# Kernel optimization log

Measured on AMD Instinct MI355X. Metric: run time of the kernel, lower is better.

## Reference

```python
import jax, jax.numpy as jnp
import numpy as np

B, T, F = 8192, 30, 16
H1, H2 = 64, 32


def _lstm(x, Wih, Whh, b):
    """PyTorch-convention LSTM (gate order i,f,g,o). x: [B,T,I] -> (ys [B,T,H], hT [B,H])."""
    H = Whh.shape[1]
    h0 = jnp.zeros((x.shape[0], H), x.dtype)

    def step(carry, xt):
        h, c = carry
        z = xt @ Wih.T + h @ Whh.T + b  # [B,4H]
        i, f, g, o = jnp.split(z, 4, axis=-1)
        c = jax.nn.sigmoid(f) * c + jax.nn.sigmoid(i) * jnp.tanh(g)
        h = jax.nn.sigmoid(o) * jnp.tanh(c)
        return (h, c), h

    (hT, _), ys = jax.lax.scan(step, (h0, h0), jnp.swapaxes(x, 0, 1))
    return jnp.swapaxes(ys, 0, 1), hT


def setup_inputs() -> dict:
    key = jax.random.key(0)
    ks = jax.random.split(key, 16)
    s = 0.1  # small init scale for numerical sanity
    return {
        "x": jax.random.normal(ks[0], (B, T, F), jnp.float32),
        "Wih1": jax.random.normal(ks[1], (4 * H1, F), jnp.float32) * s,
        "Whh1": jax.random.normal(ks[2], (4 * H1, H1), jnp.float32) * s,
        "b1": jax.random.normal(ks[3], (4 * H1,), jnp.float32) * s,
        "Wih2": jax.random.normal(ks[4], (4 * H2, H1), jnp.float32) * s,
        "Whh2": jax.random.normal(ks[5], (4 * H2, H2), jnp.float32) * s,
        "b2": jax.random.normal(ks[6], (4 * H2,), jnp.float32) * s,
        "Wih3": jax.random.normal(ks[7], (4 * H2, H2), jnp.float32) * s,
        "Whh3": jax.random.normal(ks[8], (4 * H2, H2), jnp.float32) * s,
        "b3": jax.random.normal(ks[9], (4 * H2,), jnp.float32) * s,
        "Wih4": jax.random.normal(ks[10], (4 * H1, H2), jnp.float32) * s,
        "Whh4": jax.random.normal(ks[11], (4 * H1, H1), jnp.float32) * s,
        "b4": jax.random.normal(ks[12], (4 * H1,), jnp.float32) * s,
        "Wout": jax.random.normal(ks[13], (F, H1), jnp.float32) * s,
        "bout": jax.random.normal(ks[14], (F,), jnp.float32) * s,
    }


def reference(x, Wih1, Whh1, b1, Wih2, Whh2, b2, Wih3, Whh3, b3, Wih4, Whh4, b4, Wout, bout):
    ys1, _ = _lstm(x, Wih1, Whh1, b1)          # encoder LSTM(64)
    _, latent = _lstm(ys1, Wih2, Whh2, b2)      # encoder LSTM(32) -> final hidden [B,32]
    repeated = jnp.broadcast_to(latent[:, None, :], (latent.shape[0], T, latent.shape[1]))
    ys3, _ = _lstm(repeated, Wih3, Whh3, b3)    # decoder LSTM(32)
    ys4, _ = _lstm(ys3, Wih4, Whh4, b4)         # decoder LSTM(64)
    return ys4 @ Wout.T + bout                  # [B,T,F]
```

## Files before the change

### kernel.cpp

```cpp
#include <hip/hip_runtime.h>


#define TT 30
#define FF 16
#define NT 768

typedef unsigned short u16t;
typedef __attribute__((ext_vector_type(8))) short short8;
typedef __attribute__((ext_vector_type(4))) short short4v;
typedef __attribute__((ext_vector_type(4))) float floatx4;

#define MFMA(a, b, c) __builtin_amdgcn_mfma_f32_16x16x32_bf16(a, b, c, 0, 0, 0)

#if __has_builtin(__builtin_amdgcn_exp2f)
#define EXP2(x) __builtin_amdgcn_exp2f(x)
#else
#define EXP2(x) exp2f(x)
#endif

template <int P> struct IC { static constexpr int v = P; };

__device__ __forceinline__ float rcpf(float v) { return __builtin_amdgcn_rcpf(v); }
__device__ __forceinline__ u16t f2bf(float f) {
  unsigned int u = __float_as_uint(f);
  u = (u + 0x7FFFu + ((u >> 16) & 1u)) >> 16;
  return (u16t)u;
}
__device__ __forceinline__ short8 ldFragS(const float* p, float s) {
  const float4 lo = *(const float4*)p;
  const float4 hi = *(const float4*)(p + 4);
  short8 r;
  r[0] = (short)f2bf(lo.x * s); r[1] = (short)f2bf(lo.y * s);
  r[2] = (short)f2bf(lo.z * s); r[3] = (short)f2bf(lo.w * s);
  r[4] = (short)f2bf(hi.x * s); r[5] = (short)f2bf(hi.y * s);
  r[6] = (short)f2bf(hi.z * s); r[7] = (short)f2bf(hi.w * s);
  return r;
}
__device__ __forceinline__ float cellUp(const floatx4 acc, float& c) {
  float ei = EXP2(-acc[0]);
  float ef = EXP2(-acc[1]);
  float eg = EXP2(-acc[2]);
  float eo = EXP2(-acc[3]);
  float fv = rcpf(1.f + ef);
  float P  = (1.f - eg) * rcpf((1.f + ei) * (1.f + eg));
  c = fv * c + P;
  float ec = EXP2(-2.885390082f * c);
  return (1.f - ec) * rcpf((1.f + eo) * (1.f + ec));
}

__global__ __launch_bounds__(NT, 3) void lstm_ae_mfma8(
    const float* __restrict__ x,
    const float* __restrict__ Wih1, const float* __restrict__ Whh1, const float* __restrict__ b1,
    const float* __restrict__ Wih2, const float* __restrict__ Whh2, const float* __restrict__ b2,
    const float* __restrict__ Wih3, const float* __restrict__ Whh3, const float* __restrict__ b3,
    const float* __restrict__ Wih4, const float* __restrict__ Whh4, const float* __restrict__ b4,
    const float* __restrict__ Wout, const float* __restrict__ bout,
    float* __restrict__ out)
{
  __shared__ __align__(16) u16t xAll[32 * 968];
  __shared__ __align__(16) u16t aB[32 * 264];

  const int t = threadIdx.x;
  const int w = t >> 6, lane = t & 63;
  const int q = lane >> 4, n = lane & 15;
  const int q8 = q * 8;
  const int bBase = blockIdx.x * 32;
  const int nlo = n >> 2, ngt = n & 3;
  const int r0 = n * 264, r1 = (n + 16) * 264;
  const int x0 = n * 968, x1 = (n + 16) * 968;
  const bool isZ1 = (w < 8);
  const int u = w & 3;

  const float L1 = 1.442695041f, L2 = 2.885390082f;
  const float sA = (ngt == 2) ? L2 : L1;

  for (int i = t; i < 32 * 264; i += NT) aB[i] = 0;
  {
    const float* xb = x + (size_t)bBase * (TT * FF);
    for (int i4 = t; i4 < 3840; i4 += NT) {
      int e = i4 * 4;
      int b = e / 480, r = e - b * 480;
      int stp = r >> 4, f = r & 15;
      float4 v = *(const float4*)&xb[e];
      short4v s4 = { (short)f2bf(v.x), (short)f2bf(v.y), (short)f2bf(v.z), (short)f2bf(v.w) };
      *(short4v*)&xAll[b * 968 + stp * 32 + f] = s4;
    }
    for (int i = t; i < 15360; i += NT) {
      int b = i / 480, r = i - b * 480;
      int stp = r >> 4, f = r & 15;
      xAll[b * 968 + stp * 32 + 16 + f] = 0;
    }
  }
  const short8 z8 = { 0, 0, 0, 0, 0, 0, 0, 0 };
  short8 wAf[2][3]; floatx4 biasA[2];
  if (isZ1) {
#pragma unroll
    for (int tt = 0; tt < 2; ++tt) {
      int T = w + 8 * tt;
      int row = ngt * 64 + T * 4 + nlo;
      wAf[tt][0] = z8;
      if (q < 2) wAf[tt][0] = ldFragS(&Wih1[row * 16 + q8], sA);
      wAf[tt][1] = ldFragS(&Whh1[row * 64 + q8], sA);
      wAf[tt][2] = ldFragS(&Whh1[row * 64 + 32 + q8], sA);
#pragma unroll
      for (int r = 0; r < 4; ++r) biasA[tt][r] = b1[r * 64 + T * 4 + q] * (r == 2 ? L2 : L1);
    }
  } else {
#pragma unroll
    for (int tt = 0; tt < 2; ++tt) {
      int T = 2 * u + tt;
      int row = ngt * 32 + T * 4 + nlo;
      wAf[tt][0] = ldFragS(&Wih2[row * 64 + q8], sA);
      wAf[tt][1] = ldFragS(&Wih2[row * 64 + 32 + q8], sA);
      wAf[tt][2] = ldFragS(&Whh2[row * 32 + q8], sA);
#pragma unroll
      for (int r = 0; r < 4; ++r) biasA[tt][r] = b2[r * 32 + T * 4 + q] * (r == 2 ? L2 : L1);
    }
  }
  __syncthreads();

  float cA[2][2] = {{0.f, 0.f}, {0.f, 0.f}};
  short8 bxN[2];

  if (isZ1) {
    const short8 bx0 = *(const short8*)&xAll[x0 + q8];
    const short8 bx1 = *(const short8*)&xAll[x1 + q8];
#pragma unroll
    for (int tt = 0; tt < 2; ++tt) {
      floatx4 a0 = biasA[tt], a1 = biasA[tt];
      a0 = MFMA(wAf[tt][0], bx0, a0);
      a1 = MFMA(wAf[tt][0], bx1, a1);
      aB[r0 + (w + 8 * tt) * 4 + q] = f2bf(cellUp(a0, cA[0][tt]));
      aB[r1 + (w + 8 * tt) * 4 + q] = f2bf(cellUp(a1, cA[1][tt]));
    }
    bxN[0] = *(const short8*)&xAll[x0 + 32 + q8];
    bxN[1] = *(const short8*)&xAll[x1 + 32 + q8];
  }
  __syncthreads();

  auto stepA = [&](int st, auto pc) {
    constexpr int p = decltype(pc)::v;
    const short8 h1a0 = *(const short8*)&aB[r0 + p * 64 + q8];
    const short8 h1b0 = *(const short8*)&aB[r0 + p * 64 + 32 + q8];
    const short8 h1a1 = *(const short8*)&aB[r1 + p * 64 + q8];
    const short8 h1b1 = *(const short8*)&aB[r1 + p * 64 + 32 + q8];
    if (isZ1) {
#pragma unroll
      for (int tt = 0; tt < 2; ++tt) {
        floatx4 a0 = biasA[tt], a1 = biasA[tt];
        a0 = MFMA(wAf[tt][0], bxN[0], a0);
        a1 = MFMA(wAf[tt][0], bxN[1], a1);
        a0 = MFMA(wAf[tt][1], h1a0, a0);
        a1 = MFMA(wAf[tt][1], h1a1, a1);
        a0 = MFMA(wAf[tt][2], h1b0, a0);
        a1 = MFMA(wAf[tt][2], h1b1, a1);
        aB[r0 + (1 - p) * 64 + (w + 8 * tt) * 4 + q] = f2bf(cellUp(a0, cA[0][tt]));
        aB[r1 + (1 - p) * 64 + (w + 8 * tt) * 4 + q] = f2bf(cellUp(a1, cA[1][tt]));
      }
      const int nx = (st + 2 < TT) ? st + 2 : TT - 1;
      bxN[0] = *(const short8*)&xAll[x0 + nx * 32 + q8];
      bxN[1] = *(const short8*)&xAll[x1 + nx * 32 + q8];
    } else {
      const short8 h20 = *(const short8*)&aB[r0 + 128 + (1 - p) * 32 + q8];
      const short8 h21 = *(const short8*)&aB[r1 + 128 + (1 - p) * 32 + q8];
#pragma unroll
      for (int tt = 0; tt < 2; ++tt) {
        floatx4 a0 = biasA[tt], a1 = biasA[tt];
        a0 = MFMA(wAf[tt][0], h1a0, a0);
        a1 = MFMA(wAf[tt][0], h1a1, a1);
        a0 = MFMA(wAf[tt][1], h1b0, a0);
        a1 = MFMA(wAf[tt][1], h1b1, a1);
        a0 = MFMA(wAf[tt][2], h20, a0);
        a1 = MFMA(wAf[tt][2], h21, a1);
        aB[r0 + 128 + p * 32 + (2 * u + tt) * 4 + q] = f2bf(cellUp(a0, cA[0][tt]));
        aB[r1 + 128 + p * 32 + (2 * u + tt) * 4 + q] = f2bf(cellUp(a1, cA[1][tt]));
      }
    }
    __syncthreads();
  };
  for (int st = 0; st < 28; st += 2) { stepA(st, IC<0>{}); stepA(st + 1, IC<1>{}); }
  stepA(28, IC<0>{});
  if (!isZ1) {
    const short8 h1a0 = *(const short8*)&aB[r0 + 64 + q8];
    const short8 h1b0 = *(const short8*)&aB[r0 + 96 + q8];
    const short8 h1a1 = *(const short8*)&aB[r1 + 64 + q8];
    const short8 h1b1 = *(const short8*)&aB[r1 + 96 + q8];
    const short8 h20  = *(const short8*)&aB[r0 + 128 + q8];
    const short8 h21  = *(const short8*)&aB[r1 + 128 + q8];
#pragma unroll
    for (int tt = 0; tt < 2; ++tt) {
      floatx4 a0 = biasA[tt], a1 = biasA[tt];
      a0 = MFMA(wAf[tt][0], h1a0, a0);
      a1 = MFMA(wAf[tt][0], h1a1, a1);
      a0 = MFMA(wAf[tt][1], h1b0, a0);
      a1 = MFMA(wAf[tt][1], h1b1, a1);
      a0 = MFMA(wAf[tt][2], h20, a0);
      a1 = MFMA(wAf[tt][2], h21, a1);
      aB[r0 + 160 + (2 * u + tt) * 4 + q] = f2bf(cellUp(a0, cA[0][tt]));
      aB[r1 + 160 + (2 * u + tt) * 4 + q] = f2bf(cellUp(a1, cA[1][tt]));
    }
  }
  __syncthreads();

  short8 wBf[2][3]; floatx4 biasB[2];
  short8 wof[2]; floatx4 biasO;
  short8 blat[2];
  if (isZ1) {
#pragma unroll
    for (int tt = 0; tt < 2; ++tt) {
      int T = w + 8 * tt;
      int row = ngt * 64 + T * 4 + nlo;
      wBf[tt][0] = ldFragS(&Wih4[row * 32 + q8], sA);
      wBf[tt][1] = ldFragS(&Whh4[row * 64 + q8], sA);
      wBf[tt][2] = ldFragS(&Whh4[row * 64 + 32 + q8], sA);
#pragma unroll
      for (int r = 0; r < 4; ++r) biasB[tt][r] = b4[r * 64 + T * 4 + q] * (r == 2 ? L2 : L1);
    }
    wof[0] = ldFragS(&Wout[n * 64 + q8], 1.f);
    wof[1] = ldFragS(&Wout[n * 64 + 32 + q8], 1.f);
    biasO = *(const floatx4*)&bout[q * 4];
  } else {
#pragma unroll
    for (int tt = 0; tt < 2; ++tt) {
      int T = 2 * u + tt;
      int row = ngt * 32 + T * 4 + nlo;
      wBf[tt][0] = ldFragS(&Wih3[row * 32 + q8], sA);
      wBf[tt][1] = ldFragS(&Whh3[row * 32 + q8], sA);
#pragma unroll
      for (int r = 0; r < 4; ++r) biasB[tt][r] = b3[r * 32 + T * 4 + q] * (r == 2 ? L2 : L1);
    }
    blat[0] = *(const short8*)&aB[r0 + 160 + q8];
    blat[1] = *(const short8*)&aB[r1 + 160 + q8];
  }
  for (int i = t; i < 2048; i += NT) aB[(i >> 6) * 264 + 64 + (i & 63)] = 0;
  __syncthreads();

  float cB[2][2] = {{0.f, 0.f}, {0.f, 0.f}};

  if (!isZ1) {
#pragma unroll
    for (int tt = 0; tt < 2; ++tt) {
      floatx4 a0 = biasB[tt], a1 = biasB[tt];
      a0 = MFMA(wBf[tt][0], blat[0], a0);
      a1 = MFMA(wBf[tt][0], blat[1], a1);
      aB[r0 + 192 + (2 * u + tt) * 4 + q] = f2bf(cellUp(a0, cB[0][tt]));
      aB[r1 + 192 + (2 * u + tt) * 4 + q] = f2bf(cellUp(a1, cB[1][tt]));
    }
  }
  __syncthreads();

  auto stepB = [&](int st, auto pc) {
    constexpr int p = decltype(pc)::v;
    const short8 h30 = *(const short8*)&aB[r0 + 192 + p * 32 + q8];
    const short8 h31 = *(const short8*)&aB[r1 + 192 + p * 32 + q8];
    if (isZ1) {
      const short8 h4a0 = *(const short8*)&aB[r0 + (1 - p) * 64 + q8];
      const short8 h4b0 = *(const short8*)&aB[r0 + (1 - p) * 64 + 32 + q8];
      const short8 h4a1 = *(const short8*)&aB[r1 + (1 - p) * 64 + q8];
      const short8 h4b1 = *(const short8*)&aB[r1 + (1 - p) * 64 + 32 + q8];
#pragma unroll
      for (int tt = 0; tt < 2; ++tt) {
        floatx4 a0 = biasB[tt], a1 = biasB[tt];
        a0 = MFMA(wBf[tt][0], h30, a0);
        a1 = MFMA(wBf[tt][0], h31, a1);
        a0 = MFMA(wBf[tt][1], h4a0, a0);
        a1 = MFMA(wBf[tt][1], h4a1, a1);
        a0 = MFMA(wBf[tt][2], h4b0, a0);
        a1 = MFMA(wBf[tt][2], h4b1, a1);
        aB[r0 + p * 64 + (w + 8 * tt) * 4 + q] = f2bf(cellUp(a0, cB[0][tt]));
        aB[r1 + p * 64 + (w + 8 * tt) * 4 + q] = f2bf(cellUp(a1, cB[1][tt]));
      }
      if (st > 0 && w == ((st - 1) & 7)) {
        floatx4 y0 = biasO, y1 = biasO;
        y0 = MFMA(wof[0], h4a0, y0);
        y1 = MFMA(wof[0], h4a1, y1);
        y0 = MFMA(wof[1], h4b0, y0);
        y1 = MFMA(wof[1], h4b1, y1);
        *(floatx4*)&out[((size_t)(bBase + n) * TT + (st - 1)) * FF + q * 4] = y0;
        *(floatx4*)&out[((size_t)(bBase + n + 16) * TT + (st - 1)) * FF + q * 4] = y1;
      }
    } else {
#pragma unroll
      for (int tt = 0; tt < 2; ++tt) {
        floatx4 a0 = biasB[tt], a1 = biasB[tt];
        a0 = MFMA(wBf[tt][0], blat[0], a0);
        a1 = MFMA(wBf[tt][0], blat[1], a1);
        a0 = MFMA(wBf[tt][1], h30, a0);
        a1 = MFMA(wBf[tt][1], h31, a1);
        aB[r0 + 192 + (1 - p) * 32 + (2 * u + tt) * 4 + q] = f2bf(cellUp(a0, cB[0][tt]));
        aB[r1 + 192 + (1 - p) * 32 + (2 * u + tt) * 4 + q] = f2bf(cellUp(a1, cB[1][tt]));
      }
    }
    __syncthreads();
  };
  for (int st = 0; st < 28; st += 2) { stepB(st, IC<0>{}); stepB(st + 1, IC<1>{}); }
  stepB(28, IC<0>{});
  if (isZ1) {
    const short8 h30  = *(const short8*)&aB[r0 + 224 + q8];
    const short8 h31  = *(const short8*)&aB[r1 + 224 + q8];
    const short8 h4a0 = *(const short8*)&aB[r0 + q8];
    const short8 h4b0 = *(const short8*)&aB[r0 + 32 + q8];
    const short8 h4a1 = *(const short8*)&aB[r1 + q8];
    const short8 h4b1 = *(const short8*)&aB[r1 + 32 + q8];
#pragma unroll
    for (int tt = 0; tt < 2; ++tt) {
      floatx4 a0 = biasB[tt], a1 = biasB[tt];
      a0 = MFMA(wBf[tt][0], h30, a0);
      a1 = MFMA(wBf[tt][0], h31, a1);
      a0 = MFMA(wBf[tt][1], h4a0, a0);
      a1 = MFMA(wBf[tt][1], h4a1, a1);
      a0 = MFMA(wBf[tt][2], h4b0, a0);
      a1 = MFMA(wBf[tt][2], h4b1, a1);
      aB[r0 + 64 + (w + 8 * tt) * 4 + q] = f2bf(cellUp(a0, cB[0][tt]));
      aB[r1 + 64 + (w + 8 * tt) * 4 + q] = f2bf(cellUp(a1, cB[1][tt]));
    }
    if (w == 4) {
      floatx4 y0 = biasO, y1 = biasO;
      y0 = MFMA(wof[0], h4a0, y0);
      y1 = MFMA(wof[0], h4a1, y1);
      y0 = MFMA(wof[1], h4b0, y0);
      y1 = MFMA(wof[1], h4b1, y1);
      *(floatx4*)&out[((size_t)(bBase + n) * TT + 28) * FF + q * 4] = y0;
      *(floatx4*)&out[((size_t)(bBase + n + 16) * TT + 28) * FF + q * 4] = y1;
    }
  }
  __syncthreads();
  if (w == 5) {
    const short8 ba0 = *(const short8*)&aB[r0 + 64 + q8];
    const short8 bb0 = *(const short8*)&aB[r0 + 96 + q8];
    const short8 ba1 = *(const short8*)&aB[r1 + 64 + q8];
    const short8 bb1 = *(const short8*)&aB[r1 + 96 + q8];
    floatx4 y0 = biasO, y1 = biasO;
    y0 = MFMA(wof[0], ba0, y0);
    y1 = MFMA(wof[0], ba1, y1);
    y0 = MFMA(wof[1], bb0, y0);
    y1 = MFMA(wof[1], bb1, y1);
    *(floatx4*)&out[((size_t)(bBase + n) * TT + 29) * FF + q * 4] = y0;
    *(floatx4*)&out[((size_t)(bBase + n + 16) * TT + 29) * FF + q * 4] = y1;
  }
}

extern "C" void kernel_launch(void* const* d_in, const int* in_sizes, int n_in,
                              void* d_out, int out_size, void* d_ws, size_t ws_size,
                              hipStream_t stream) {
  const float* x    = (const float*)d_in[0];
  const float* Wih1 = (const float*)d_in[1];
  const float* Whh1 = (const float*)d_in[2];
  const float* b1   = (const float*)d_in[3];
  const float* Wih2 = (const float*)d_in[4];
  const float* Whh2 = (const float*)d_in[5];
  const float* b2   = (const float*)d_in[6];
  const float* Wih3 = (const float*)d_in[7];
  const float* Whh3 = (const float*)d_in[8];
  const float* b3   = (const float*)d_in[9];
  const float* Wih4 = (const float*)d_in[10];
  const float* Whh4 = (const float*)d_in[11];
  const float* b4   = (const float*)d_in[12];
  const float* Wout = (const float*)d_in[13];
  const float* bout = (const float*)d_in[14];
  float* out = (float*)d_out;

  const int B = in_sizes[0] / (TT * FF);
  dim3 grid(B / 32), block(NT);
  lstm_ae_mfma8<<<grid, block, 0, stream>>>(
      x, Wih1, Whh1, b1, Wih2, Whh2, b2, Wih3, Whh3, b3,
      Wih4, Whh4, b4, Wout, bout, out);
}
```

Before: 159.7 us.

## Halve batch per block and give each wave four gate tiles instead of two

Each block now handles 16 batch rows with 6 waves (384 threads) instead of 32 rows with 12 waves. Each wave computes four 16-row gate tiles against a single batch fragment, where before it computed two tiles against two batch fragments. The grid doubles and shared memory per block halves, so more blocks fit per CU and each barrier covers fewer waves. The cost is that every wave now holds twice as many weight fragments, which raises register pressure, and weight-fragment reuse across batch fragments is lost, so more MFMA issues are needed per batch row.

```diff
diff --git a/kernel.cpp b/kernel.cpp
--- a/kernel.cpp
+++ b/kernel.cpp
@@ -3,7 +3,7 @@
 
 #define TT 30
 #define FF 16
-#define NT 768
+#define NT 384
 
 typedef unsigned short u16t;
 typedef __attribute__((ext_vector_type(8))) short short8;
@@ -48,7 +48,7 @@
   return (1.f - ec) * rcpf((1.f + eo) * (1.f + ec));
 }
 
-__global__ __launch_bounds__(NT, 3) void lstm_ae_mfma8(
+__global__ __launch_bounds__(NT, 3) void lstm_ae_mfma9(
     const float* __restrict__ x,
     const float* __restrict__ Wih1, const float* __restrict__ Whh1, const float* __restrict__ b1,
     const float* __restrict__ Wih2, const float* __restrict__ Whh2, const float* __restrict__ b2,
@@ -57,27 +57,27 @@
     const float* __restrict__ Wout, const float* __restrict__ bout,
     float* __restrict__ out)
 {
-  __shared__ __align__(16) u16t xAll[32 * 968];
-  __shared__ __align__(16) u16t aB[32 * 264];
+  __shared__ __align__(16) u16t xAll[16 * 968];
+  __shared__ __align__(16) u16t aB[16 * 264];
 
   const int t = threadIdx.x;
   const int w = t >> 6, lane = t & 63;
   const int q = lane >> 4, n = lane & 15;
   const int q8 = q * 8;
-  const int bBase = blockIdx.x * 32;
+  const int bBase = blockIdx.x * 16;
   const int nlo = n >> 2, ngt = n & 3;
-  const int r0 = n * 264, r1 = (n + 16) * 264;
-  const int x0 = n * 968, x1 = (n + 16) * 968;
-  const bool isZ1 = (w < 8);
-  const int u = w & 3;
+  const int r0 = n * 264;
+  const int x0 = n * 968;
+  const bool isZ1 = (w < 4);
+  const int u = w & 1;
 
   const float L1 = 1.442695041f, L2 = 2.885390082f;
   const float sA = (ngt == 2) ? L2 : L1;
 
-  for (int i = t; i < 32 * 264; i += NT) aB[i] = 0;
+  for (int i = t; i < 16 * 264; i += NT) aB[i] = 0;
   {
     const float* xb = x + (size_t)bBase * (TT * FF);
-    for (int i4 = t; i4 < 3840; i4 += NT) {
+    for (int i4 = t; i4 < 1920; i4 += NT) {
       int e = i4 * 4;
       int b = e / 480, r = e - b * 480;
       int stp = r >> 4, f = r & 15;
@@ -85,18 +85,18 @@
       short4v s4 = { (short)f2bf(v.x), (short)f2bf(v.y), (short)f2bf(v.z), (short)f2bf(v.w) };
       *(short4v*)&xAll[b * 968 + stp * 32 + f] = s4;
     }
-    for (int i = t; i < 15360; i += NT) {
+    for (int i = t; i < 7680; i += NT) {
       int b = i / 480, r = i - b * 480;
       int stp = r >> 4, f = r & 15;
       xAll[b * 968 + stp * 32 + 16 + f] = 0;
     }
   }
   const short8 z8 = { 0, 0, 0, 0, 0, 0, 0, 0 };
-  short8 wAf[2][3]; floatx4 biasA[2];
+  short8 wAf[4][3]; floatx4 biasA[4];
   if (isZ1) {
 #pragma unroll
-    for (int tt = 0; tt < 2; ++tt) {
-      int T = w + 8 * tt;
+    for (int tt = 0; tt < 4; ++tt) {
+      int T = w + 4 * tt;
       int row = ngt * 64 + T * 4 + nlo;
       wAf[tt][0] = z8;
       if (q < 2) wAf[tt][0] = ldFragS(&Wih1[row * 16 + q8], sA);
@@ -107,8 +107,8 @@
     }
   } else {
 #pragma unroll
-    for (int tt = 0; tt < 2; ++tt) {
-      int T = 2 * u + tt;
+    for (int tt = 0; tt < 4; ++tt) {
+      int T = 4 * u + tt;
       int row = ngt * 32 + T * 4 + nlo;
       wAf[tt][0] = ldFragS(&Wih2[row * 64 + q8], sA);
       wAf[tt][1] = ldFragS(&Wih2[row * 64 + 32 + q8], sA);
@@ -119,61 +119,45 @@
   }
   __syncthreads();
 
-  float cA[2][2] = {{0.f, 0.f}, {0.f, 0.f}};
-  short8 bxN[2];
+  float cA[4] = {0.f, 0.f, 0.f, 0.f};
+  short8 bxN;
 
   if (isZ1) {
     const short8 bx0 = *(const short8*)&xAll[x0 + q8];
-    const short8 bx1 = *(const short8*)&xAll[x1 + q8];
-#pragma unroll
-    for (int tt = 0; tt < 2; ++tt) {
-      floatx4 a0 = biasA[tt], a1 = biasA[tt];
-      a0 = MFMA(wAf[tt][0], bx0, a0);
-      a1 = MFMA(wAf[tt][0], bx1, a1);
-      aB[r0 + (w + 8 * tt) * 4 + q] = f2bf(cellUp(a0, cA[0][tt]));
-      aB[r1 + (w + 8 * tt) * 4 + q] = f2bf(cellUp(a1, cA[1][tt]));
-    }
-    bxN[0] = *(const short8*)&xAll[x0 + 32 + q8];
-    bxN[1] = *(const short8*)&xAll[x1 + 32 + q8];
+#pragma unroll
+    for (int tt = 0; tt < 4; ++tt) {
+      floatx4 a = biasA[tt];
+      a = MFMA(wAf[tt][0], bx0, a);
+      aB[r0 + (w + 4 * tt) * 4 + q] = f2bf(cellUp(a, cA[tt]));
+    }
+    bxN = *(const short8*)&xAll[x0 + 32 + q8];
   }
   __syncthreads();
 
   auto stepA = [&](int st, auto pc) {
     constexpr int p = decltype(pc)::v;
-    const short8 h1a0 = *(const short8*)&aB[r0 + p * 64 + q8];
-    const short8 h1b0 = *(const short8*)&aB[r0 + p * 64 + 32 + q8];
-    const short8 h1a1 = *(const short8*)&aB[r1 + p * 64 + q8];
-    const short8 h1b1 = *(const short8*)&aB[r1 + p * 64 + 32 + q8];
+    const short8 h1a = *(const short8*)&aB[r0 + p * 64 + q8];
+    const short8 h1b = *(const short8*)&aB[r0 + p * 64 + 32 + q8];
     if (isZ1) {
 #pragma unroll
-      for (int tt = 0; tt < 2; ++tt) {
-        floatx4 a0 = biasA[tt], a1 = biasA[tt];
-        a0 = MFMA(wAf[tt][0], bxN[0], a0);
-        a1 = MFMA(wAf[tt][0], bxN[1], a1);
-        a0 = MFMA(wAf[tt][1], h1a0, a0);
-        a1 = MFMA(wAf[tt][1], h1a1, a1);
-        a0 = MFMA(wAf[tt][2], h1b0, a0);
-        a1 = MFMA(wAf[tt][2], h1b1, a1);
-        aB[r0 + (1 - p) * 64 + (w + 8 * tt) * 4 + q] = f2bf(cellUp(a0, cA[0][tt]));
-        aB[r1 + (1 - p) * 64 + (w + 8 * tt) * 4 + q] = f2bf(cellUp(a1, cA[1][tt]));
+      for (int tt = 0; tt < 4; ++tt) {
+        floatx4 a = biasA[tt];
+        a = MFMA(wAf[tt][0], bxN, a);
+        a = MFMA(wAf[tt][1], h1a, a);
+        a = MFMA(wAf[tt][2], h1b, a);
+        aB[r0 + (1 - p) * 64 + (w + 4 * tt) * 4 + q] = f2bf(cellUp(a, cA[tt]));
       }
       const int nx = (st + 2 < TT) ? st + 2 : TT - 1;
-      bxN[0] = *(const short8*)&xAll[x0 + nx * 32 + q8];
-      bxN[1] = *(const short8*)&xAll[x1 + nx * 32 + q8];
+      bxN = *(const short8*)&xAll[x0 + nx * 32 + q8];
     } else {
-      const short8 h20 = *(const short8*)&aB[r0 + 128 + (1 - p) * 32 + q8];
-      const short8 h21 = *(const short8*)&aB[r1 + 128 + (1 - p) * 32 + q8];
-#pragma unroll
-      for (int tt = 0; tt < 2; ++tt) {
-        floatx4 a0 = biasA[tt], a1 = biasA[tt];
-        a0 = MFMA(wAf[tt][0], h1a0, a0);
-        a1 = MFMA(wAf[tt][0], h1a1, a1);
-        a0 = MFMA(wAf[tt][1], h1b0, a0);
-        a1 = MFMA(wAf[tt][1], h1b1, a1);
-        a0 = MFMA(wAf[tt][2], h20, a0);
-        a1 = MFMA(wAf[tt][2], h21, a1);
-        aB[r0 + 128 + p * 32 + (2 * u + tt) * 4 + q] = f2bf(cellUp(a0, cA[0][tt]));
-        aB[r1 + 128 + p * 32 + (2 * u + tt) * 4 + q] = f2bf(cellUp(a1, cA[1][tt]));
+      const short8 h2 = *(const short8*)&aB[r0 + 128 + (1 - p) * 32 + q8];
+#pragma unroll
+      for (int tt = 0; tt < 4; ++tt) {
+        floatx4 a = biasA[tt];
+        a = MFMA(wAf[tt][0], h1a, a);
+        a = MFMA(wAf[tt][1], h1b, a);
+        a = MFMA(wAf[tt][2], h2, a);
+        aB[r0 + 128 + p * 32 + (4 * u + tt) * 4 + q] = f2bf(cellUp(a, cA[tt]));
       }
     }
     __syncthreads();
@@ -181,34 +165,27 @@
   for (int st = 0; st < 28; st += 2) { stepA(st, IC<0>{}); stepA(st + 1, IC<1>{}); }
   stepA(28, IC<0>{});
   if (!isZ1) {
-    const short8 h1a0 = *(const short8*)&aB[r0 + 64 + q8];
-    const short8 h1b0 = *(const short8*)&aB[r0 + 96 + q8];
-    const short8 h1a1 = *(const short8*)&aB[r1 + 64 + q8];
-    const short8 h1b1 = *(const short8*)&aB[r1 + 96 + q8];
-    const short8 h20  = *(const short8*)&aB[r0 + 128 + q8];
-    const short8 h21  = *(const short8*)&aB[r1 + 128 + q8];
-#pragma unroll
-    for (int tt = 0; tt < 2; ++tt) {
-      floatx4 a0 = biasA[tt], a1 = biasA[tt];
-      a0 = MFMA(wAf[tt][0], h1a0, a0);
-      a1 = MFMA(wAf[tt][0], h1a1, a1);
-      a0 = MFMA(wAf[tt][1], h1b0, a0);
-      a1 = MFMA(wAf[tt][1], h1b1, a1);
-      a0 = MFMA(wAf[tt][2], h20, a0);
-      a1 = MFMA(wAf[tt][2], h21, a1);
-      aB[r0 + 160 + (2 * u + tt) * 4 + q] = f2bf(cellUp(a0, cA[0][tt]));
-      aB[r1 + 160 + (2 * u + tt) * 4 + q] = f2bf(cellUp(a1, cA[1][tt]));
-    }
-  }
-  __syncthreads();
-
-  short8 wBf[2][3]; floatx4 biasB[2];
+    const short8 h1a = *(const short8*)&aB[r0 + 64 + q8];
+    const short8 h1b = *(const short8*)&aB[r0 + 96 + q8];
+    const short8 h2  = *(const short8*)&aB[r0 + 128 + q8];
+#pragma unroll
+    for (int tt = 0; tt < 4; ++tt) {
+      floatx4 a = biasA[tt];
+      a = MFMA(wAf[tt][0], h1a, a);
+      a = MFMA(wAf[tt][1], h1b, a);
+      a = MFMA(wAf[tt][2], h2, a);
+      aB[r0 + 160 + (4 * u + tt) * 4 + q] = f2bf(cellUp(a, cA[tt]));
+    }
+  }
+  __syncthreads();
+
+  short8 wBf[4][3]; floatx4 biasB[4];
   short8 wof[2]; floatx4 biasO;
-  short8 blat[2];
+  short8 blat;
   if (isZ1) {
 #pragma unroll
-    for (int tt = 0; tt < 2; ++tt) {
-      int T = w + 8 * tt;
+    for (int tt = 0; tt < 4; ++tt) {
+      int T = w + 4 * tt;
       int row = ngt * 64 + T * 4 + nlo;
       wBf[tt][0] = ldFragS(&Wih4[row * 32 + q8], sA);
       wBf[tt][1] = ldFragS(&Whh4[row * 64 + q8], sA);
@@ -221,74 +198,58 @@
     biasO = *(const floatx4*)&bout[q * 4];
   } else {
 #pragma unroll
-    for (int tt = 0; tt < 2; ++tt) {
-      int T = 2 * u + tt;
+    for (int tt = 0; tt < 4; ++tt) {
+      int T = 4 * u + tt;
       int row = ngt * 32 + T * 4 + nlo;
       wBf[tt][0] = ldFragS(&Wih3[row * 32 + q8], sA);
       wBf[tt][1] = ldFragS(&Whh3[row * 32 + q8], sA);
 #pragma unroll
       for (int r = 0; r < 4; ++r) biasB[tt][r] = b3[r * 32 + T * 4 + q] * (r == 2 ? L2 : L1);
     }
-    blat[0] = *(const short8*)&aB[r0 + 160 + q8];
-    blat[1] = *(const short8*)&aB[r1 + 160 + q8];
-  }
-  for (int i = t; i < 2048; i += NT) aB[(i >> 6) * 264 + 64 + (i & 63)] = 0;
-  __syncthreads();
-
-  float cB[2][2] = {{0.f, 0.f}, {0.f, 0.f}};
+    blat = *(const short8*)&aB[r0 + 160 + q8];
+  }
+  for (int i = t; i < 1024; i += NT) aB[(i >> 6) * 264 + 64 + (i & 63)] = 0;
+  __syncthreads();
+
+  float cB[4] = {0.f, 0.f, 0.f, 0.f};
 
   if (!isZ1) {
 #pragma unroll
-    for (int tt = 0; tt < 2; ++tt) {
-      floatx4 a0 = biasB[tt], a1 = biasB[tt];
-      a0 = MFMA(wBf[tt][0], blat[0], a0);
-      a1 = MFMA(wBf[tt][0], blat[1], a1);
-      aB[r0 + 192 + (2 * u + tt) * 4 + q] = f2bf(cellUp(a0, cB[0][tt]));
-      aB[r1 + 192 + (2 * u + tt) * 4 + q] = f2bf(cellUp(a1, cB[1][tt]));
+    for (int tt = 0; tt < 4; ++tt) {
+      floatx4 a = biasB[tt];
+      a = MFMA(wBf[tt][0], blat, a);
+      aB[r0 + 192 + (4 * u + tt) * 4 + q] = f2bf(cellUp(a, cB[tt]));
     }
   }
   __syncthreads();
 
   auto stepB = [&](int st, auto pc) {
     constexpr int p = decltype(pc)::v;
-    const short8 h30 = *(const short8*)&aB[r0 + 192 + p * 32 + q8];
-    const short8 h31 = *(const short8*)&aB[r1 + 192 + p * 32 + q8];
+    const short8 h3 = *(const short8*)&aB[r0 + 192 + p * 32 + q8];
     if (isZ1) {
-      const short8 h4a0 = *(const short8*)&aB[r0 + (1 - p) * 64 + q8];
-      const short8 h4b0 = *(const short8*)&aB[r0 + (1 - p) * 64 + 32 + q8];
-      const short8 h4a1 = *(const short8*)&aB[r1 + (1 - p) * 64 + q8];
-      const short8 h4b1 = *(const short8*)&aB[r1 + (1 - p) * 64 + 32 + q8];
-#pragma unroll
-      for (int tt = 0; tt < 2; ++tt) {
-        floatx4 a0 = biasB[tt], a1 = biasB[tt];
-        a0 = MFMA(wBf[tt][0], h30, a0);
-        a1 = MFMA(wBf[tt][0], h31, a1);
-        a0 = MFMA(wBf[tt][1], h4a0, a0);
-        a1 = MFMA(wBf[tt][1], h4a1, a1);
-        a0 = MFMA(wBf[tt][2], h4b0, a0);
-        a1 = MFMA(wBf[tt][2], h4b1, a1);
-        aB[r0 + p * 64 + (w + 8 * tt) * 4 + q] = f2bf(cellUp(a0, cB[0][tt]));
-        aB[r1 + p * 64 + (w + 8 * tt) * 4 + q] = f2bf(cellUp(a1, cB[1][tt]));
-      }
-      if (st > 0 && w == ((st - 1) & 7)) {
-        floatx4 y0 = biasO, y1 = biasO;
-        y0 = MFMA(wof[0], h4a0, y0);
-        y1 = MFMA(wof[0], h4a1, y1);
-        y0 = MFMA(wof[1], h4b0, y0);
-        y1 = MFMA(wof[1], h4b1, y1);
-        *(floatx4*)&out[((size_t)(bBase + n) * TT + (st - 1)) * FF + q * 4] = y0;
-        *(floatx4*)&out[((size_t)(bBase + n + 16) * TT + (st - 1)) * FF + q * 4] = y1;
+      const short8 h4a = *(const short8*)&aB[r0 + (1 - p) * 64 + q8];
+      const short8 h4b = *(const short8*)&aB[r0 + (1 - p) * 64 + 32 + q8];
+#pragma unroll
+      for (int tt = 0; tt < 4; ++tt) {
+        floatx4 a = biasB[tt];
+        a = MFMA(wBf[tt][0], h3, a);
+        a = MFMA(wBf[tt][1], h4a, a);
+        a = MFMA(wBf[tt][2], h4b, a);
+        aB[r0 + p * 64 + (w + 4 * tt) * 4 + q] = f2bf(cellUp(a, cB[tt]));
+      }
+      if (st > 0 && w == ((st - 1) & 3)) {
+        floatx4 y = biasO;
+        y = MFMA(wof[0], h4a, y);
+        y = MFMA(wof[1], h4b, y);
+        *(floatx4*)&out[((size_t)(bBase + n) * TT + (st - 1)) * FF + q * 4] = y;
       }
     } else {
 #pragma unroll
-      for (int tt = 0; tt < 2; ++tt) {
-        floatx4 a0 = biasB[tt], a1 = biasB[tt];
-        a0 = MFMA(wBf[tt][0], blat[0], a0);
-        a1 = MFMA(wBf[tt][0], blat[1], a1);
-        a0 = MFMA(wBf[tt][1], h30, a0);
-        a1 = MFMA(wBf[tt][1], h31, a1);
-        aB[r0 + 192 + (1 - p) * 32 + (2 * u + tt) * 4 + q] = f2bf(cellUp(a0, cB[0][tt]));
-        aB[r1 + 192 + (1 - p) * 32 + (2 * u + tt) * 4 + q] = f2bf(cellUp(a1, cB[1][tt]));
+      for (int tt = 0; tt < 4; ++tt) {
+        floatx4 a = biasB[tt];
+        a = MFMA(wBf[tt][0], blat, a);
+        a = MFMA(wBf[tt][1], h3, a);
+        aB[r0 + 192 + (1 - p) * 32 + (4 * u + tt) * 4 + q] = f2bf(cellUp(a, cB[tt]));
       }
     }
     __syncthreads();
@@ -296,47 +257,32 @@
   for (int st = 0; st < 28; st += 2) { stepB(st, IC<0>{}); stepB(st + 1, IC<1>{}); }
   stepB(28, IC<0>{});
   if (isZ1) {
-    const short8 h30  = *(const short8*)&aB[r0 + 224 + q8];
-    const short8 h31  = *(const short8*)&aB[r1 + 224 + q8];
-    const short8 h4a0 = *(const short8*)&aB[r0 + q8];
-    const short8 h4b0 = *(const short8*)&aB[r0 + 32 + q8];
-    const short8 h4a1 = *(const short8*)&aB[r1 + q8];
-    const short8 h4b1 = *(const short8*)&aB[r1 + 32 + q8];
-#pragma unroll
-    for (int tt = 0; tt < 2; ++tt) {
-      floatx4 a0 = biasB[tt], a1 = biasB[tt];
-      a0 = MFMA(wBf[tt][0], h30, a0);
-      a1 = MFMA(wBf[tt][0], h31, a1);
-      a0 = MFMA(wBf[tt][1], h4a0, a0);
-      a1 = MFMA(wBf[tt][1], h4a1, a1);
-      a0 = MFMA(wBf[tt][2], h4b0, a0);
-      a1 = MFMA(wBf[tt][2], h4b1, a1);
-      aB[r0 + 64 + (w + 8 * tt) * 4 + q] = f2bf(cellUp(a0, cB[0][tt]));
-      aB[r1 + 64 + (w + 8 * tt) * 4 + q] = f2bf(cellUp(a1, cB[1][tt]));
-    }
-    if (w == 4) {
-      floatx4 y0 = biasO, y1 = biasO;
-      y0 = MFMA(wof[0], h4a0, y0);
-      y1 = MFMA(wof[0], h4a1, y1);
-      y0 = MFMA(wof[1], h4b0, y0);
-      y1 = MFMA(wof[1], h4b1, y1);
-      *(floatx4*)&out[((size_t)(bBase + n) * TT + 28) * FF + q * 4] = y0;
-      *(floatx4*)&out[((size_t)(bBase + n + 16) * TT + 28) * FF + q * 4] = y1;
-    }
-  }
-  __syncthreads();
-  if (w == 5) {
-    const short8 ba0 = *(const short8*)&aB[r0 + 64 + q8];
-    const short8 bb0 = *(const short8*)&aB[r0 + 96 + q8];
-    const short8 ba1 = *(const short8*)&aB[r1 + 64 + q8];
-    const short8 bb1 = *(const short8*)&aB[r1 + 96 + q8];
-    floatx4 y0 = biasO, y1 = biasO;
-    y0 = MFMA(wof[0], ba0, y0);
-    y1 = MFMA(wof[0], ba1, y1);
-    y0 = MFMA(wof[1], bb0, y0);
-    y1 = MFMA(wof[1], bb1, y1);
-    *(floatx4*)&out[((size_t)(bBase + n) * TT + 29) * FF + q * 4] = y0;
-    *(floatx4*)&out[((size_t)(bBase + n + 16) * TT + 29) * FF + q * 4] = y1;
+    const short8 h3  = *(const short8*)&aB[r0 + 224 + q8];
+    const short8 h4a = *(const short8*)&aB[r0 + q8];
+    const short8 h4b = *(const short8*)&aB[r0 + 32 + q8];
+#pragma unroll
+    for (int tt = 0; tt < 4; ++tt) {
+      floatx4 a = biasB[tt];
+      a = MFMA(wBf[tt][0], h3, a);
+      a = MFMA(wBf[tt][1], h4a, a);
+      a = MFMA(wBf[tt][2], h4b, a);
+      aB[r0 + 64 + (w + 4 * tt) * 4 + q] = f2bf(cellUp(a, cB[tt]));
+    }
+    if (w == 0) {
+      floatx4 y = biasO;
+      y = MFMA(wof[0], h4a, y);
+      y = MFMA(wof[1], h4b, y);
+      *(floatx4*)&out[((size_t)(bBase + n) * TT + 28) * FF + q * 4] = y;
+    }
+  }
+  __syncthreads();
+  if (w == 1) {
+    const short8 ba = *(const short8*)&aB[r0 + 64 + q8];
+    const short8 bb = *(const short8*)&aB[r0 + 96 + q8];
+    floatx4 y = biasO;
+    y = MFMA(wof[0], ba, y);
+    y = MFMA(wof[1], bb, y);
+    *(floatx4*)&out[((size_t)(bBase + n) * TT + 29) * FF + q * 4] = y;
   }
 }
 
@@ -361,8 +307,8 @@
   float* out = (float*)d_out;
 
   const int B = in_sizes[0] / (TT * FF);
-  dim3 grid(B / 32), block(NT);
-  lstm_ae_mfma8<<<grid, block, 0, stream>>>(
+  dim3 grid(B / 16), block(NT);
+  lstm_ae_mfma9<<<grid, block, 0, stream>>>(
       x, Wih1, Whh1, b1, Wih2, Whh2, b2, Wih3, Whh3, b3,
       Wih4, Whh4, b4, Wout, bout, out);
 }
```

New measurement: 192.0 us. +20.3%, slower.

## Give every wave both layer roles with 16 waves per block

Applied to the files above, without the earlier changes.

The block grows from 12 to 16 waves and the split into specialized layer-1 and layer-2 waves is removed. Each wave now computes one 4-unit tile of the 64-wide layer and one half-batch tile of the 32-wide layer on every step, so the work per wave is uniform and divergent branches disappear. The decoder's constant input projection (Wih3 times latent plus bias) is computed once before the loop and reused as the accumulator seed. In exchange, more threads share each block barrier, and at the declared 4 blocks per CU the register budget per thread is tighter, which could cause spills.

```diff
diff --git a/kernel.cpp b/kernel.cpp
--- a/kernel.cpp
+++ b/kernel.cpp
@@ -3,7 +3,7 @@
 
 #define TT 30
 #define FF 16
-#define NT 768
+#define NT 1024
 
 typedef unsigned short u16t;
 typedef __attribute__((ext_vector_type(8))) short short8;
@@ -48,7 +48,7 @@
   return (1.f - ec) * rcpf((1.f + eo) * (1.f + ec));
 }
 
-__global__ __launch_bounds__(NT, 3) void lstm_ae_mfma8(
+__global__ __launch_bounds__(NT, 4) void lstm_ae_mfma10(
     const float* __restrict__ x,
     const float* __restrict__ Wih1, const float* __restrict__ Whh1, const float* __restrict__ b1,
     const float* __restrict__ Wih2, const float* __restrict__ Whh2, const float* __restrict__ b2,
@@ -68,8 +68,8 @@
   const int nlo = n >> 2, ngt = n & 3;
   const int r0 = n * 264, r1 = (n + 16) * 264;
   const int x0 = n * 968, x1 = (n + 16) * 968;
-  const bool isZ1 = (w < 8);
-  const int u = w & 3;
+  const int tz = w >> 1, hz = w & 1;
+  const int rz = hz ? r1 : r0;
 
   const float L1 = 1.442695041f, L2 = 2.885390082f;
   const float sA = (ngt == 2) ? L2 : L1;
@@ -92,47 +92,38 @@
     }
   }
   const short8 z8 = { 0, 0, 0, 0, 0, 0, 0, 0 };
-  short8 wAf[2][3]; floatx4 biasA[2];
-  if (isZ1) {
+  short8 w1f[3]; floatx4 bias1;
+  {
+    int row = ngt * 64 + w * 4 + nlo;
+    w1f[0] = z8;
+    if (q < 2) w1f[0] = ldFragS(&Wih1[row * 16 + q8], sA);
+    w1f[1] = ldFragS(&Whh1[row * 64 + q8], sA);
+    w1f[2] = ldFragS(&Whh1[row * 64 + 32 + q8], sA);
 #pragma unroll
-    for (int tt = 0; tt < 2; ++tt) {
-      int T = w + 8 * tt;
-      int row = ngt * 64 + T * 4 + nlo;
-      wAf[tt][0] = z8;
-      if (q < 2) wAf[tt][0] = ldFragS(&Wih1[row * 16 + q8], sA);
-      wAf[tt][1] = ldFragS(&Whh1[row * 64 + q8], sA);
-      wAf[tt][2] = ldFragS(&Whh1[row * 64 + 32 + q8], sA);
+    for (int r = 0; r < 4; ++r) bias1[r] = b1[r * 64 + w * 4 + q] * (r == 2 ? L2 : L1);
+  }
+  short8 w2f[3]; floatx4 bias2;
+  {
+    int row = ngt * 32 + tz * 4 + nlo;
+    w2f[0] = ldFragS(&Wih2[row * 64 + q8], sA);
+    w2f[1] = ldFragS(&Wih2[row * 64 + 32 + q8], sA);
+    w2f[2] = ldFragS(&Whh2[row * 32 + q8], sA);
 #pragma unroll
-      for (int r = 0; r < 4; ++r) biasA[tt][r] = b1[r * 64 + T * 4 + q] * (r == 2 ? L2 : L1);
-    }
-  } else {
-#pragma unroll
-    for (int tt = 0; tt < 2; ++tt) {
-      int T = 2 * u + tt;
-      int row = ngt * 32 + T * 4 + nlo;
-      wAf[tt][0] = ldFragS(&Wih2[row * 64 + q8], sA);
-      wAf[tt][1] = ldFragS(&Wih2[row * 64 + 32 + q8], sA);
-      wAf[tt][2] = ldFragS(&Whh2[row * 32 + q8], sA);
-#pragma unroll
-      for (int r = 0; r < 4; ++r) biasA[tt][r] = b2[r * 32 + T * 4 + q] * (r == 2 ? L2 : L1);
-    }
-  }
-  __syncthreads();
-
-  float cA[2][2] = {{0.f, 0.f}, {0.f, 0.f}};
+    for (int r = 0; r < 4; ++r) bias2[r] = b2[r * 32 + tz * 4 + q] * (r == 2 ? L2 : L1);
+  }
+  __syncthreads();
+
+  float cA[3] = {0.f, 0.f, 0.f};
   short8 bxN[2];
 
-  if (isZ1) {
+  {
     const short8 bx0 = *(const short8*)&xAll[x0 + q8];
     const short8 bx1 = *(const short8*)&xAll[x1 + q8];
-#pragma unroll
-    for (int tt = 0; tt < 2; ++tt) {
-      floatx4 a0 = biasA[tt], a1 = biasA[tt];
-      a0 = MFMA(wAf[tt][0], bx0, a0);
-      a1 = MFMA(wAf[tt][0], bx1, a1);
-      aB[r0 + (w + 8 * tt) * 4 + q] = f2bf(cellUp(a0, cA[0][tt]));
-      aB[r1 + (w + 8 * tt) * 4 + q] = f2bf(cellUp(a1, cA[1][tt]));
-    }
+    floatx4 a0 = bias1, a1 = bias1;
+    a0 = MFMA(w1f[0], bx0, a0);
+    a1 = MFMA(w1f[0], bx1, a1);
+    aB[r0 + w * 4 + q] = f2bf(cellUp(a0, cA[0]));
+    aB[r1 + w * 4 + q] = f2bf(cellUp(a1, cA[1]));
     bxN[0] = *(const short8*)&xAll[x0 + 32 + q8];
     bxN[1] = *(const short8*)&xAll[x1 + 32 + q8];
   }
@@ -144,177 +135,124 @@
     const short8 h1b0 = *(const short8*)&aB[r0 + p * 64 + 32 + q8];
     const short8 h1a1 = *(const short8*)&aB[r1 + p * 64 + q8];
     const short8 h1b1 = *(const short8*)&aB[r1 + p * 64 + 32 + q8];
-    if (isZ1) {
-#pragma unroll
-      for (int tt = 0; tt < 2; ++tt) {
-        floatx4 a0 = biasA[tt], a1 = biasA[tt];
-        a0 = MFMA(wAf[tt][0], bxN[0], a0);
-        a1 = MFMA(wAf[tt][0], bxN[1], a1);
-        a0 = MFMA(wAf[tt][1], h1a0, a0);
-        a1 = MFMA(wAf[tt][1], h1a1, a1);
-        a0 = MFMA(wAf[tt][2], h1b0, a0);
-        a1 = MFMA(wAf[tt][2], h1b1, a1);
-        aB[r0 + (1 - p) * 64 + (w + 8 * tt) * 4 + q] = f2bf(cellUp(a0, cA[0][tt]));
-        aB[r1 + (1 - p) * 64 + (w + 8 * tt) * 4 + q] = f2bf(cellUp(a1, cA[1][tt]));
-      }
-      const int nx = (st + 2 < TT) ? st + 2 : TT - 1;
-      bxN[0] = *(const short8*)&xAll[x0 + nx * 32 + q8];
-      bxN[1] = *(const short8*)&xAll[x1 + nx * 32 + q8];
-    } else {
-      const short8 h20 = *(const short8*)&aB[r0 + 128 + (1 - p) * 32 + q8];
-      const short8 h21 = *(const short8*)&aB[r1 + 128 + (1 - p) * 32 + q8];
-#pragma unroll
-      for (int tt = 0; tt < 2; ++tt) {
-        floatx4 a0 = biasA[tt], a1 = biasA[tt];
-        a0 = MFMA(wAf[tt][0], h1a0, a0);
-        a1 = MFMA(wAf[tt][0], h1a1, a1);
-        a0 = MFMA(wAf[tt][1], h1b0, a0);
-        a1 = MFMA(wAf[tt][1], h1b1, a1);
-        a0 = MFMA(wAf[tt][2], h20, a0);
-        a1 = MFMA(wAf[tt][2], h21, a1);
-        aB[r0 + 128 + p * 32 + (2 * u + tt) * 4 + q] = f2bf(cellUp(a0, cA[0][tt]));
-        aB[r1 + 128 + p * 32 + (2 * u + tt) * 4 + q] = f2bf(cellUp(a1, cA[1][tt]));
-      }
-    }
+    const short8 h1az = *(const short8*)&aB[rz + p * 64 + q8];
+    const short8 h1bz = *(const short8*)&aB[rz + p * 64 + 32 + q8];
+    const short8 h2z  = *(const short8*)&aB[rz + 128 + (1 - p) * 32 + q8];
+    floatx4 a0 = bias1, a1 = bias1;
+    a0 = MFMA(w1f[0], bxN[0], a0);
+    a1 = MFMA(w1f[0], bxN[1], a1);
+    a0 = MFMA(w1f[1], h1a0, a0);
+    a1 = MFMA(w1f[1], h1a1, a1);
+    a0 = MFMA(w1f[2], h1b0, a0);
+    a1 = MFMA(w1f[2], h1b1, a1);
+    floatx4 a2 = bias2;
+    a2 = MFMA(w2f[0], h1az, a2);
+    a2 = MFMA(w2f[1], h1bz, a2);
+    a2 = MFMA(w2f[2], h2z, a2);
+    aB[r0 + (1 - p) * 64 + w * 4 + q] = f2bf(cellUp(a0, cA[0]));
+    aB[r1 + (1 - p) * 64 + w * 4 + q] = f2bf(cellUp(a1, cA[1]));
+    aB[rz + 128 + p * 32 + tz * 4 + q] = f2bf(cellUp(a2, cA[2]));
+    const int nx = (st + 2 < TT) ? st + 2 : TT - 1;
+    bxN[0] = *(const short8*)&xAll[x0 + nx * 32 + q8];
+    bxN[1] = *(const short8*)&xAll[x1 + nx * 32 + q8];
     __syncthreads();
   };
   for (int st = 0; st < 28; st += 2) { stepA(st, IC<0>{}); stepA(st + 1, IC<1>{}); }
   stepA(28, IC<0>{});
-  if (!isZ1) {
-    const short8 h1a0 = *(const short8*)&aB[r0 + 64 + q8];
-    const short8 h1b0 = *(const short8*)&aB[r0 + 96 + q8];
-    const short8 h1a1 = *(const short8*)&aB[r1 + 64 + q8];
-    const short8 h1b1 = *(const short8*)&aB[r1 + 96 + q8];
-    const short8 h20  = *(const short8*)&aB[r0 + 128 + q8];
-    const short8 h21  = *(const short8*)&aB[r1 + 128 + q8];
+  {
+    const short8 h1az = *(const short8*)&aB[rz + 64 + q8];
+    const short8 h1bz = *(const short8*)&aB[rz + 96 + q8];
+    const short8 h2z  = *(const short8*)&aB[rz + 128 + q8];
+    floatx4 a2 = bias2;
+    a2 = MFMA(w2f[0], h1az, a2);
+    a2 = MFMA(w2f[1], h1bz, a2);
+    a2 = MFMA(w2f[2], h2z, a2);
+    aB[rz + 160 + tz * 4 + q] = f2bf(cellUp(a2, cA[2]));
+  }
+  __syncthreads();
+
+  short8 w4f[3]; floatx4 bias4;
+  {
+    int row = ngt * 64 + w * 4 + nlo;
+    w4f[0] = ldFragS(&Wih4[row * 32 + q8], sA);
+    w4f[1] = ldFragS(&Whh4[row * 64 + q8], sA);
+    w4f[2] = ldFragS(&Whh4[row * 64 + 32 + q8], sA);
 #pragma unroll
-    for (int tt = 0; tt < 2; ++tt) {
-      floatx4 a0 = biasA[tt], a1 = biasA[tt];
-      a0 = MFMA(wAf[tt][0], h1a0, a0);
-      a1 = MFMA(wAf[tt][0], h1a1, a1);
-      a0 = MFMA(wAf[tt][1], h1b0, a0);
-      a1 = MFMA(wAf[tt][1], h1b1, a1);
-      a0 = MFMA(wAf[tt][2], h20, a0);
-      a1 = MFMA(wAf[tt][2], h21, a1);
-      aB[r0 + 160 + (2 * u + tt) * 4 + q] = f2bf(cellUp(a0, cA[0][tt]));
-      aB[r1 + 160 + (2 * u + tt) * 4 + q] = f2bf(cellUp(a1, cA[1][tt]));
-    }
-  }
-  __syncthreads();
-
-  short8 wBf[2][3]; floatx4 biasB[2];
+    for (int r = 0; r < 4; ++r) bias4[r] = b4[r * 64 + w * 4 + q] * (r == 2 ? L2 : L1);
+  }
+  short8 w3h; floatx4 acc3c;
+  {
+    int row = ngt * 32 + tz * 4 + nlo;
+    const short8 w3i = ldFragS(&Wih3[row * 32 + q8], sA);
+    w3h = ldFragS(&Whh3[row * 32 + q8], sA);
+    floatx4 b3v;
+#pragma unroll
+    for (int r = 0; r < 4; ++r) b3v[r] = b3[r * 32 + tz * 4 + q] * (r == 2 ? L2 : L1);
+    const short8 blat = *(const short8*)&aB[rz + 160 + q8];
+    acc3c = MFMA(w3i, blat, b3v);
+  }
   short8 wof[2]; floatx4 biasO;
-  short8 blat[2];
-  if (isZ1) {
-#pragma unroll
-    for (int tt = 0; tt < 2; ++tt) {
-      int T = w + 8 * tt;
-      int row = ngt * 64 + T * 4 + nlo;
-      wBf[tt][0] = ldFragS(&Wih4[row * 32 + q8], sA);
-      wBf[tt][1] = ldFragS(&Whh4[row * 64 + q8], sA);
-      wBf[tt][2] = ldFragS(&Whh4[row * 64 + 32 + q8], sA);
-#pragma unroll
-      for (int r = 0; r < 4; ++r) biasB[tt][r] = b4[r * 64 + T * 4 + q] * (r == 2 ? L2 : L1);
-    }
-    wof[0] = ldFragS(&Wout[n * 64 + q8], 1.f);
-    wof[1] = ldFragS(&Wout[n * 64 + 32 + q8], 1.f);
-    biasO = *(const floatx4*)&bout[q * 4];
-  } else {
-#pragma unroll
-    for (int tt = 0; tt < 2; ++tt) {
-      int T = 2 * u + tt;
-      int row = ngt * 32 + T * 4 + nlo;
-      wBf[tt][0] = ldFragS(&Wih3[row * 32 + q8], sA);
-      wBf[tt][1] = ldFragS(&Whh3[row * 32 + q8], sA);
-#pragma unroll
-      for (int r = 0; r < 4; ++r) biasB[tt][r] = b3[r * 32 + T * 4 + q] * (r == 2 ? L2 : L1);
-    }
-    blat[0] = *(const short8*)&aB[r0 + 160 + q8];
-    blat[1] = *(const short8*)&aB[r1 + 160 + q8];
-  }
+  wof[0] = ldFragS(&Wout[n * 64 + q8], 1.f);
+  wof[1] = ldFragS(&Wout[n * 64 + 32 + q8], 1.f);
+  biasO = *(const floatx4*)&bout[q * 4];
   for (int i = t; i < 2048; i += NT) aB[(i >> 6) * 264 + 64 + (i & 63)] = 0;
   __syncthreads();
 
-  float cB[2][2] = {{0.f, 0.f}, {0.f, 0.f}};
-
-  if (!isZ1) {
-#pragma unroll
-    for (int tt = 0; tt < 2; ++tt) {
-      floatx4 a0 = biasB[tt], a1 = biasB[tt];
-      a0 = MFMA(wBf[tt][0], blat[0], a0);
-      a1 = MFMA(wBf[tt][0], blat[1], a1);
-      aB[r0 + 192 + (2 * u + tt) * 4 + q] = f2bf(cellUp(a0, cB[0][tt]));
-      aB[r1 + 192 + (2 * u + tt) * 4 + q] = f2bf(cellUp(a1, cB[1][tt]));
-    }
-  }
+  float cB[3] = {0.f, 0.f, 0.f};
+
+  aB[rz + 192 + tz * 4 + q] = f2bf(cellUp(acc3c, cB[2]));
   __syncthreads();
 
   auto stepB = [&](int st, auto pc) {
     constexpr int p = decltype(pc)::v;
-    const short8 h30 = *(const short8*)&aB[r0 + 192 + p * 32 + q8];
-    const short8 h31 = *(const short8*)&aB[r1 + 192 + p * 32 + q8];
-    if (isZ1) {
-      const short8 h4a0 = *(const short8*)&aB[r0 + (1 - p) * 64 + q8];
-      const short8 h4b0 = *(const short8*)&aB[r0 + (1 - p) * 64 + 32 + q8];
-      const short8 h4a1 = *(const short8*)&aB[r1 + (1 - p) * 64 + q8];
-      const short8 h4b1 = *(const short8*)&aB[r1 + (1 - p) * 64 + 32 + q8];
-#pragma unroll
-      for (int tt = 0; tt < 2; ++tt) {
-        floatx4 a0 = biasB[tt], a1 = biasB[tt];
-        a0 = MFMA(wBf[tt][0], h30, a0);
-        a1 = MFMA(wBf[tt][0], h31, a1);
-        a0 = MFMA(wBf[tt][1], h4a0, a0);
-        a1 = MFMA(wBf[tt][1], h4a1, a1);
-        a0 = MFMA(wBf[tt][2], h4b0, a0);
-        a1 = MFMA(wBf[tt][2], h4b1, a1);
-        aB[r0 + p * 64 + (w + 8 * tt) * 4 + q] = f2bf(cellUp(a0, cB[0][tt]));
-        aB[r1 + p * 64 + (w + 8 * tt) * 4 + q] = f2bf(cellUp(a1, cB[1][tt]));
-      }
-      if (st > 0 && w == ((st - 1) & 7)) {
-        floatx4 y0 = biasO, y1 = biasO;
-        y0 = MFMA(wof[0], h4a0, y0);
-        y1 = MFMA(wof[0], h4a1, y1);
-        y0 = MFMA(wof[1], h4b0, y0);
-        y1 = MFMA(wof[1], h4b1, y1);
-        *(floatx4*)&out[((size_t)(bBase + n) * TT + (st - 1)) * FF + q * 4] = y0;
-        *(floatx4*)&out[((size_t)(bBase + n + 16) * TT + (st - 1)) * FF + q * 4] = y1;
-      }
-    } else {
-#pragma unroll
-      for (int tt = 0; tt < 2; ++tt) {
-        floatx4 a0 = biasB[tt], a1 = biasB[tt];
-        a0 = MFMA(wBf[tt][0], blat[0], a0);
-        a1 = MFMA(wBf[tt][0], blat[1], a1);
-        a0 = MFMA(wBf[tt][1], h30, a0);
-        a1 = MFMA(wBf[tt][1], h31, a1);
-        aB[r0 + 192 + (1 - p) * 32 + (2 * u + tt) * 4 + q] = f2bf(cellUp(a0, cB[0][tt]));
-        aB[r1 + 192 + (1 - p) * 32 + (2 * u + tt) * 4 + q] = f2bf(cellUp(a1, cB[1][tt]));
-      }
+    const short8 h4a0 = *(const short8*)&aB[r0 + (1 - p) * 64 + q8];
+    const short8 h4b0 = *(const short8*)&aB[r0 + (1 - p) * 64 + 32 + q8];
+    const short8 h4a1 = *(const short8*)&aB[r1 + (1 - p) * 64 + q8];
+    const short8 h4b1 = *(const short8*)&aB[r1 + (1 - p) * 64 + 32 + q8];
+    const short8 h30  = *(const short8*)&aB[r0 + 192 + p * 32 + q8];
+    const short8 h31  = *(const short8*)&aB[r1 + 192 + p * 32 + q8];
+    const short8 h3z  = *(const short8*)&aB[rz + 192 + p * 32 + q8];
+    floatx4 a0 = bias4, a1 = bias4;
+    a0 = MFMA(w4f[0], h30, a0);
+    a1 = MFMA(w4f[0], h31, a1);
+    a0 = MFMA(w4f[1], h4a0, a0);
+    a1 = MFMA(w4f[1], h4a1, a1);
+    a0 = MFMA(w4f[2], h4b0, a0);
+    a1 = MFMA(w4f[2], h4b1, a1);
+    floatx4 a2 = MFMA(w3h, h3z, acc3c);
+    aB[r0 + p * 64 + w * 4 + q] = f2bf(cellUp(a0, cB[0]));
+    aB[r1 + p * 64 + w * 4 + q] = f2bf(cellUp(a1, cB[1]));
+    aB[rz + 192 + (1 - p) * 32 + tz * 4 + q] = f2bf(cellUp(a2, cB[2]));
+    if (st > 0 && w == ((st - 1) & 15)) {
+      floatx4 y0 = biasO, y1 = biasO;
+      y0 = MFMA(wof[0], h4a0, y0);
+      y1 = MFMA(wof[0], h4a1, y1);
+      y0 = MFMA(wof[1], h4b0, y0);
+      y1 = MFMA(wof[1], h4b1, y1);
+      *(floatx4*)&out[((size_t)(bBase + n) * TT + (st - 1)) * FF + q * 4] = y0;
+      *(floatx4*)&out[((size_t)(bBase + n + 16) * TT + (st - 1)) * FF + q * 4] = y1;
     }
     __syncthreads();
   };
   for (int st = 0; st < 28; st += 2) { stepB(st, IC<0>{}); stepB(st + 1, IC<1>{}); }
   stepB(28, IC<0>{});
-  if (isZ1) {
+  {
     const short8 h30  = *(const short8*)&aB[r0 + 224 + q8];
     const short8 h31  = *(const short8*)&aB[r1 + 224 + q8];
     const short8 h4a0 = *(const short8*)&aB[r0 + q8];
     const short8 h4b0 = *(const short8*)&aB[r0 + 32 + q8];
     const short8 h4a1 = *(const short8*)&aB[r1 + q8];
     const short8 h4b1 = *(const short8*)&aB[r1 + 32 + q8];
-#pragma unroll
-    for (int tt = 0; tt < 2; ++tt) {
-      floatx4 a0 = biasB[tt], a1 = biasB[tt];
-      a0 = MFMA(wBf[tt][0], h30, a0);
-      a1 = MFMA(wBf[tt][0], h31, a1);
-      a0 = MFMA(wBf[tt][1], h4a0, a0);
-      a1 = MFMA(wBf[tt][1], h4a1, a1);
-      a0 = MFMA(wBf[tt][2], h4b0, a0);
-      a1 = MFMA(wBf[tt][2], h4b1, a1);
-      aB[r0 + 64 + (w + 8 * tt) * 4 + q] = f2bf(cellUp(a0, cB[0][tt]));
-      aB[r1 + 64 + (w + 8 * tt) * 4 + q] = f2bf(cellUp(a1, cB[1][tt]));
-    }
-    if (w == 4) {
+    floatx4 a0 = bias4, a1 = bias4;
+    a0 = MFMA(w4f[0], h30, a0);
+    a1 = MFMA(w4f[0], h31, a1);
+    a0 = MFMA(w4f[1], h4a0, a0);
+    a1 = MFMA(w4f[1], h4a1, a1);
+    a0 = MFMA(w4f[2], h4b0, a0);
+    a1 = MFMA(w4f[2], h4b1, a1);
+    aB[r0 + 64 + w * 4 + q] = f2bf(cellUp(a0, cB[0]));
+    aB[r1 + 64 + w * 4 + q] = f2bf(cellUp(a1, cB[1]));
+    if (w == 12) {
       floatx4 y0 = biasO, y1 = biasO;
       y0 = MFMA(wof[0], h4a0, y0);
       y1 = MFMA(wof[0], h4a1, y1);
@@ -325,7 +263,7 @@
     }
   }
   __syncthreads();
-  if (w == 5) {
+  if (w == 13) {
     const short8 ba0 = *(const short8*)&aB[r0 + 64 + q8];
     const short8 bb0 = *(const short8*)&aB[r0 + 96 + q8];
     const short8 ba1 = *(const short8*)&aB[r1 + 64 + q8];
@@ -362,7 +300,7 @@
 
   const int B = in_sizes[0] / (TT * FF);
   dim3 grid(B / 32), block(NT);
-  lstm_ae_mfma8<<<grid, block, 0, stream>>>(
+  lstm_ae_mfma10<<<grid, block, 0, stream>>>(
       x, Wih1, Whh1, b1, Wih2, Whh2, b2, Wih3, Whh3, b3,
       Wih4, Whh4, b4, Wout, bout, out);
 }
```

Result: slower. 165.9 us (+3.9%).
